# Performance work log

Measured on AMD Instinct MI355X. Metric: run time of the kernel, lower is better.

Reference implementation:

```python
import jax, jax.numpy as jnp
import numpy as np

S_LEN, T_LEN, BATCH, HID = 32, 32, 64, 512


def setup_inputs() -> dict:
    key = jax.random.key(0)
    ks = jax.random.split(key, 5)
    H = HID
    sc = lambda n: 1.0 / np.sqrt(n)
    return {
        "source": jax.random.normal(ks[0], (S_LEN, BATCH, H), jnp.float32),
        "target": jax.random.normal(ks[1], (T_LEN, BATCH, H), jnp.float32),
        # H2h Dense: concat(s_h, t_h) [B, 2H] -> [B, H], linear
        "W_H2h": (jax.random.normal(ks[2], (2 * H, H), jnp.float32) * sc(2 * H)),
        "b_H2h": jnp.zeros((H,), jnp.float32),
        # shared LSTMCell weights (Keras gate order i, f, g, o)
        "W_kernel": (jax.random.normal(ks[3], (H, 4 * H), jnp.float32) * sc(H)),
        "W_rec": (jax.random.normal(ks[4], (H, 4 * H), jnp.float32) * sc(H)),
        "b_lstm": jnp.zeros((4 * H,), jnp.float32),
    }


def _lstm_cell(x, h, c, Wk, Wr, b):
    # Keras LSTMCell math, gate order i, f, g(candidate), o
    z = x @ Wk + h @ Wr + b  # [B, 4H]
    i, f, g, o = jnp.split(z, 4, axis=-1)
    c2 = jax.nn.sigmoid(f) * c + jax.nn.sigmoid(i) * jnp.tanh(g)
    h2 = jax.nn.sigmoid(o) * jnp.tanh(c2)
    return h2, c2


def reference(source, target, W_H2h, b_H2h, W_kernel, W_rec, b_lstm):
    # source: [S, B, H] (time-major), target: [T, B, H]
    T, B, H = target.shape

    def inner(s_state, t_slice):
        # s_state carried along the target axis; t_slice is target cell j state
        s_step, s_h, s_m = s_state
        t_step, t_h, t_m = t_slice
        hmid = jnp.concatenate([s_h, t_h], axis=1) @ W_H2h + b_H2h  # [B, H]
        ns_h, ns_m = _lstm_cell(s_step, hmid, s_m, W_kernel, W_rec, b_lstm)
        nt_h, nt_m = _lstm_cell(t_step, hmid, t_m, W_kernel, W_rec, b_lstm)
        # step arrays get overwritten with the new hidden state
        return (ns_h, ns_h, ns_m), (nt_h, nt_h, nt_m)

    def outer(t_arrays, s_in):
        # fresh source state per outer step i: step = source[i], h = m = 0
        z = jnp.zeros_like(s_in)
        (s_step_f, _, _), t_new = jax.lax.scan(inner, (s_in, z, z), t_arrays)
        return t_new, s_step_f

    zeros = jnp.zeros((T, B, H), source.dtype)
    t_final, source_out = jax.lax.scan(outer, (target, zeros, zeros), source)
    return source_out, t_final[0]
```

## Files before the change

kernel.cpp:

```cpp
#include <hip/hip_runtime.h>

#define BLK 256

typedef __bf16 bf16;
typedef __bf16 bf16x8 __attribute__((ext_vector_type(8)));
typedef float f32x4 __attribute__((ext_vector_type(4)));

__device__ __forceinline__ float sigm(float x) { return 1.f / (1.f + __expf(-x)); }
__device__ __forceinline__ float tanh_(float x) {
    x = fminf(fmaxf(x, -15.f), 15.f);
    float e = __expf(2.f * x);
    return (e - 1.f) / (e + 1.f);
}

__device__ __forceinline__ void gl2lds(const bf16* g, bf16* l) {
    __builtin_amdgcn_global_load_lds((const __attribute__((address_space(1))) void*)g,
                                     (__attribute__((address_space(3))) void*)l, 16, 0, 0);
}

__global__ __launch_bounds__(256) void k_prep(
    const float* __restrict__ src, const float* __restrict__ tgt,
    const float* __restrict__ WH, const float* __restrict__ bH,
    const float* __restrict__ Wk, const float* __restrict__ Wr,
    const float* __restrict__ bl,
    bf16* __restrict__ srcb, bf16* __restrict__ tgtb,
    bf16* __restrict__ WHhi, bf16* __restrict__ WHlo,
    bf16* __restrict__ Wrhi, bf16* __restrict__ Wrlo,
    bf16* __restrict__ P2, float* __restrict__ bz) {
    __shared__ float tile[64][65];
    const int bid = blockIdx.x, t = threadIdx.x;
    if (bid < 512) {
        const float* in = (bid < 256) ? Wr : Wk;
        bf16* ohi = (bid < 256) ? Wrhi : P2;
        bf16* olo = (bid < 256) ? Wrlo : nullptr;
        const int b = bid & 255;
        const int tr = b >> 5, tc = b & 31;
#pragma unroll
        for (int q = 0; q < 16; q++) {
            int idx = q * 256 + t, lr = idx >> 6, lc = idx & 63;
            tile[lr][lc] = in[(size_t)(tr * 64 + lr) * 2048 + tc * 64 + lc];
        }
        __syncthreads();
#pragma unroll
        for (int q = 0; q < 16; q++) {
            int idx = q * 256 + t, lr = idx >> 6, lc = idx & 63;
            float v = tile[lc][lr];
            size_t o = (size_t)(tc * 64 + lr) * 512 + tr * 64 + lc;
            bf16 h = (bf16)v;
            ohi[o] = h;
            if (olo) olo[o] = (bf16)(v - (float)h);
        }
    } else if (bid < 520) {
        int c = (bid - 512) * 256 + t;
        float s = bl[c];
        for (int k = 0; k < 512; k++) s += bH[k] * Wr[(size_t)k * 2048 + c];
        bz[c] = s;
    } else {
        const int gt = (bid - 520) * 256 + t, NT = 504 * 256;
        for (int id = gt; id < 1048576; id += NT) srcb[id] = (bf16)src[id];
        for (int id = gt; id < 1048576; id += NT) tgtb[id] = (bf16)tgt[id];
        for (int id = gt; id < 524288; id += NT) {
            float v = WH[id];
            bf16 h = (bf16)v;
            WHhi[id] = h;
            WHlo[id] = (bf16)(v - (float)h);
        }
    }
}

__global__ __launch_bounds__(256, 4) void k_gemmP(
    const bf16* __restrict__ Wrhi, const bf16* __restrict__ Wrlo,
    const bf16* __restrict__ WHhi, const bf16* __restrict__ WHlo,
    const float* __restrict__ Wk,
    bf16* __restrict__ P1, bf16* __restrict__ P3,
    bf16* __restrict__ P4, bf16* __restrict__ P5) {
    __shared__ __align__(16) bf16 At[64 * 64];
    __shared__ __align__(16) bf16 Bt[128 * 64];
    const int t = threadIdx.x, w = t >> 6, l = t & 63;
    const int m0 = (blockIdx.x >> 3) * 64, n0 = (blockIdx.x & 7) * 128;
    f32x4 acc[2][4] = {};
    const bf16* Aps[3] = {Wrhi, Wrlo, Wrhi};
    const bf16* Bps[3] = {WHhi, WHhi, WHlo};
    for (int ph = 0; ph < 3; ph++) {
        const bf16* Ap = Aps[ph] + (size_t)m0 * 512;
        const bf16* Bp = Bps[ph] + (size_t)n0 * 512;
        for (int kt = 0; kt < 8; kt++) {
            int k0 = kt * 64;
            __syncthreads();
#pragma unroll
            for (int q = 0; q < 2; q++) {
                int pp = q * 256 + t;
                int r = pp >> 3, c = (pp & 7) ^ (r & 7);
                gl2lds(Ap + (size_t)r * 512 + k0 + c * 8, &At[(q * 256 + w * 64) * 8]);
            }
#pragma unroll
            for (int q = 0; q < 4; q++) {
                int pp = q * 256 + t;
                int r = pp >> 3, c = (pp & 7) ^ (r & 7);
                gl2lds(Bp + (size_t)r * 512 + k0 + c * 8, &Bt[(q * 256 + w * 64) * 8]);
            }
            __syncthreads();
#pragma unroll
            for (int ks = 0; ks < 2; ks++) {
                int c = ks * 4 + (l >> 4);
                bf16x8 af[2], bb[4];
#pragma unroll
                for (int mt = 0; mt < 2; mt++) {
                    int r = (w >> 1) * 32 + mt * 16 + (l & 15);
                    af[mt] = *(const bf16x8*)&At[(r * 8 + (c ^ (r & 7))) * 8];
                }
#pragma unroll
                for (int g = 0; g < 4; g++) {
                    int r = g * 32 + (w & 1) * 16 + (l & 15);
                    bb[g] = *(const bf16x8*)&Bt[(r * 8 + (c ^ (r & 7))) * 8];
                }
#pragma unroll
                for (int mt = 0; mt < 2; mt++)
#pragma unroll
                    for (int g = 0; g < 4; g++)
                        acc[mt][g] = __builtin_amdgcn_mfma_f32_16x16x32_bf16(
                            af[mt], bb[g], acc[mt][g], 0, 0, 0);
            }
        }
    }
    const bool hihalf = (n0 >= 512);
#pragma unroll
    for (int mt = 0; mt < 2; mt++) {
#pragma unroll
        for (int g = 0; g < 4; g++) {
            int np = n0 + g * 32 + (w & 1) * 16 + (l & 15);
#pragma unroll
            for (int r = 0; r < 4; r++) {
                int c = m0 + (w >> 1) * 32 + mt * 16 + ((l >> 4) << 2) + r;
                float v = acc[mt][g][r];
                if (!hihalf) {
                    P4[(size_t)c * 512 + np] = (bf16)v;
                    P1[(size_t)c * 512 + np] = (bf16)(v + Wk[(size_t)np * 2048 + c]);
                } else {
                    int kk = np - 512;
                    P3[(size_t)c * 512 + kk] = (bf16)v;
                    P5[(size_t)c * 512 + kk] = (bf16)(v + Wk[(size_t)kk * 2048 + c]);
                }
            }
        }
    }
}

__global__ __launch_bounds__(256, 3) void k_diag3(
    int d, int i_lo,
    const bf16* __restrict__ srcb, const bf16* __restrict__ tgtb,
    const bf16* __restrict__ P1, const bf16* __restrict__ P2,
    const bf16* __restrict__ P3, const bf16* __restrict__ P4,
    const bf16* __restrict__ P5,
    const float* __restrict__ bz,
    const bf16* __restrict__ shR, bf16* __restrict__ shW,
    const bf16* __restrict__ thR, bf16* __restrict__ thW,
    float* __restrict__ sc, float* __restrict__ tc,
    float* __restrict__ out) {
    __shared__ __align__(16) bf16 At[64 * 128];
    __shared__ __align__(16) bf16 Bt[128 * 128];
    const int t = threadIdx.x, w = t >> 6, l = t & 63;
    const int cell = blockIdx.x >> 5, sub = blockIdx.x & 31;
    const int side = sub >> 4, ch0 = (sub & 15) << 5;
    const int i = i_lo + cell, j = d - i;
    const size_t stI = (size_t)i * 32768, stJ = (size_t)j * 32768;

    const bf16* Ah[2];
    const bf16* Wh[2];
    int nh = 0;
    if (side == 0) {
        Ah[nh] = (j == 0 ? srcb : shR) + stI;
        Wh[nh] = (j == 0 ? P2 : P1);
        nh++;
        if (i > 0) { Ah[nh] = thR + stJ; Wh[nh] = P3; nh++; }
    } else {
        if (j > 0) { Ah[nh] = shR + stI; Wh[nh] = P4; nh++; }
        Ah[nh] = (i == 0 ? tgtb : thR) + stJ;
        Wh[nh] = (i == 0 ? P2 : P5);
        nh++;
    }

    f32x4 acc[2][4] = {};
    for (int hh = 0; hh < nh; hh++) {
        const bf16* Ap = Ah[hh];
        const bf16* Wp = Wh[hh];
#pragma unroll 1
        for (int kt = 0; kt < 4; kt++) {
            int k0 = kt * 128;
            __syncthreads();
#pragma unroll
            for (int q = 0; q < 4; q++) {
                int pp = q * 256 + t;
                int r = pp >> 4, c = (pp & 15) ^ (r & 15);
                gl2lds(Ap + (size_t)r * 512 + k0 + c * 8, &At[(q * 256 + w * 64) * 8]);
            }
#pragma unroll
            for (int q = 0; q < 8; q++) {
                int pp = q * 256 + t;
                int r = pp >> 4, c = (pp & 15) ^ (r & 15);
                int g = r >> 5;
                gl2lds(Wp + (size_t)(g * 512 + ch0 + (r & 31)) * 512 + k0 + c * 8,
                       &Bt[(q * 256 + w * 64) * 8]);
            }
            __syncthreads();
#pragma unroll
            for (int ks = 0; ks < 4; ks++) {
                int cq = ks * 4 + (l >> 4);
                bf16x8 af[2], bb[4];
#pragma unroll
                for (int mt = 0; mt < 2; mt++) {
                    int r = (w >> 1) * 32 + mt * 16 + (l & 15);
                    af[mt] = *(const bf16x8*)&At[(r * 16 + (cq ^ (r & 15))) * 8];
                }
#pragma unroll
                for (int g = 0; g < 4; g++) {
                    int r = g * 32 + (w & 1) * 16 + (l & 15);
                    bb[g] = *(const bf16x8*)&Bt[(r * 16 + (cq ^ (r & 15))) * 8];
                }
#pragma unroll
                for (int mt = 0; mt < 2; mt++)
#pragma unroll
                    for (int g = 0; g < 4; g++)
                        acc[mt][g] = __builtin_amdgcn_mfma_f32_16x16x32_bf16(
                            af[mt], bb[g], acc[mt][g], 0, 0, 0);
            }
        }
    }

    const int h = ch0 + (w & 1) * 16 + (l & 15);
    float bzv[4];
#pragma unroll
    for (int g = 0; g < 4; g++) bzv[g] = bz[g * 512 + h];
#pragma unroll
    for (int mt = 0; mt < 2; mt++) {
#pragma unroll
        for (int r = 0; r < 4; r++) {
            int b = (w >> 1) * 32 + mt * 16 + ((l >> 4) << 2) + r;
            float zi = acc[mt][0][r] + bzv[0];
            float zf = acc[mt][1][r] + bzv[1];
            float zg = acc[mt][2][r] + bzv[2];
            float zo = acc[mt][3][r] + bzv[3];
            if (side == 0) {
                size_t off = stI + (size_t)b * 512 + h;
                float cold = (j == 0) ? 0.f : sc[off];
                float c2 = sigm(zf) * cold + sigm(zi) * tanh_(zg);
                float h2 = sigm(zo) * tanh_(c2);
                sc[off] = c2;
                shW[off] = (bf16)h2;
                if (j == 31) out[off] = h2;
            } else {
                size_t off = stJ + (size_t)b * 512 + h;
                float cold = (i == 0) ? 0.f : tc[off];
                float c2 = sigm(zf) * cold + sigm(zi) * tanh_(zg);
                float h2 = sigm(zo) * tanh_(c2);
                tc[off] = c2;
                thW[off] = (bf16)h2;
                if (i == 31) out[1048576 + off] = h2;
            }
        }
    }
}


extern "C" void kernel_launch(void* const* d_in, const int* in_sizes, int n_in,
                              void* d_out, int out_size, void* d_ws, size_t ws_size,
                              hipStream_t stream) {
    char* w = (char*)d_ws;
    const size_t MB = 1u << 20;
    const float* src = (const float*)d_in[0];
    const float* tgt = (const float*)d_in[1];
    const float* WH = (const float*)d_in[2];
    const float* bH = (const float*)d_in[3];
    const float* Wk = (const float*)d_in[4];
    const float* Wr = (const float*)d_in[5];
    const float* bl = (const float*)d_in[6];
    float* out = (float*)d_out;

    bf16* srcb = (bf16*)(w + 0 * MB);
    bf16* tgtb = (bf16*)(w + 2 * MB);
    bf16* WHhi = (bf16*)(w + 4 * MB);
    bf16* WHlo = (bf16*)(w + 5 * MB);
    bf16* Wrhi = (bf16*)(w + 6 * MB);
    bf16* Wrlo = (bf16*)(w + 8 * MB);
    bf16* P1 = (bf16*)(w + 10 * MB);
    bf16* P2 = (bf16*)(w + 12 * MB);
    bf16* P3 = (bf16*)(w + 14 * MB);
    bf16* P4 = (bf16*)(w + 16 * MB);
    bf16* P5 = (bf16*)(w + 18 * MB);
    float* bz = (float*)(w + 20 * MB);
    bf16* sh = (bf16*)(w + 21 * MB);
    bf16* th = (bf16*)(w + 25 * MB);
    float* sc = (float*)(w + 29 * MB);
    float* tc = (float*)(w + 33 * MB);

    k_prep<<<1024, BLK, 0, stream>>>(src, tgt, WH, bH, Wk, Wr, bl, srcb, tgtb,
                                     WHhi, WHlo, Wrhi, Wrlo, P2, bz);
    k_gemmP<<<256, BLK, 0, stream>>>(Wrhi, Wrlo, WHhi, WHlo, Wk, P1, P3, P4, P5);

    for (int d = 0; d < 63; d++) {
        int i_lo = d > 31 ? d - 31 : 0;
        int i_hi = d < 31 ? d : 31;
        int Kd = i_hi - i_lo + 1;
        const bf16* shR = sh + (size_t)(d & 1) * 1048576;
        bf16* shW = sh + (size_t)((d + 1) & 1) * 1048576;
        const bf16* thR = th + (size_t)(d & 1) * 1048576;
        bf16* thW = th + (size_t)((d + 1) & 1) * 1048576;
        k_diag3<<<Kd * 32, BLK, 0, stream>>>(d, i_lo, srcb, tgtb, P1, P2, P3, P4, P5,
                                             bz, shR, shW, thR, thW, sc, tc, out);
    }
}
```

Before: 1.410 ms.

## Load A operand directly to registers and add deep-K variant for small diagonals

The diagonal kernel no longer stages the activation tile in LDS. Each wave reads its A fragments straight from global memory into registers, which cuts LDS use and raises the occupancy hint to 4. A second kernel variant uses a 256-wide K tile with a larger LDS weight buffer, so short diagonals with few blocks go through fewer K iterations and barriers. The host picks a variant per diagonal by its cell count. Direct global A loads read each row without the LDS reuse across waves, and they add register pressure.

```diff
diff --git a/kernel.cpp b/kernel.cpp
--- a/kernel.cpp
+++ b/kernel.cpp
@@ -146,88 +146,36 @@
     }
 }
 
-__global__ __launch_bounds__(256, 3) void k_diag3(
-    int d, int i_lo,
-    const bf16* __restrict__ srcb, const bf16* __restrict__ tgtb,
-    const bf16* __restrict__ P1, const bf16* __restrict__ P2,
-    const bf16* __restrict__ P3, const bf16* __restrict__ P4,
-    const bf16* __restrict__ P5,
-    const float* __restrict__ bz,
-    const bf16* __restrict__ shR, bf16* __restrict__ shW,
-    const bf16* __restrict__ thR, bf16* __restrict__ thW,
-    float* __restrict__ sc, float* __restrict__ tc,
-    float* __restrict__ out) {
-    __shared__ __align__(16) bf16 At[64 * 128];
-    __shared__ __align__(16) bf16 Bt[128 * 128];
-    const int t = threadIdx.x, w = t >> 6, l = t & 63;
-    const int cell = blockIdx.x >> 5, sub = blockIdx.x & 31;
-    const int side = sub >> 4, ch0 = (sub & 15) << 5;
-    const int i = i_lo + cell, j = d - i;
+__device__ __forceinline__ int build_panels(int i, int d, int side,
+                                            const bf16* srcb, const bf16* tgtb,
+                                            const bf16* shR, const bf16* thR,
+                                            const bf16* P1, const bf16* P2,
+                                            const bf16* P3, const bf16* P4,
+                                            const bf16* P5, const bf16** A,
+                                            const bf16** W) {
+    const int j = d - i;
     const size_t stI = (size_t)i * 32768, stJ = (size_t)j * 32768;
-
-    const bf16* Ah[2];
-    const bf16* Wh[2];
     int nh = 0;
     if (side == 0) {
-        Ah[nh] = (j == 0 ? srcb : shR) + stI;
-        Wh[nh] = (j == 0 ? P2 : P1);
+        A[nh] = (j == 0 ? srcb : shR) + stI;
+        W[nh] = (j == 0 ? P2 : P1);
         nh++;
-        if (i > 0) { Ah[nh] = thR + stJ; Wh[nh] = P3; nh++; }
+        if (i > 0) { A[nh] = thR + stJ; W[nh] = P3; nh++; }
     } else {
-        if (j > 0) { Ah[nh] = shR + stI; Wh[nh] = P4; nh++; }
-        Ah[nh] = (i == 0 ? tgtb : thR) + stJ;
-        Wh[nh] = (i == 0 ? P2 : P5);
+        if (j > 0) { A[nh] = shR + stI; W[nh] = P4; nh++; }
+        A[nh] = (i == 0 ? tgtb : thR) + stJ;
+        W[nh] = (i == 0 ? P2 : P5);
         nh++;
     }
-
-    f32x4 acc[2][4] = {};
-    for (int hh = 0; hh < nh; hh++) {
-        const bf16* Ap = Ah[hh];
-        const bf16* Wp = Wh[hh];
-#pragma unroll 1
-        for (int kt = 0; kt < 4; kt++) {
-            int k0 = kt * 128;
-            __syncthreads();
-#pragma unroll
-            for (int q = 0; q < 4; q++) {
-                int pp = q * 256 + t;
-                int r = pp >> 4, c = (pp & 15) ^ (r & 15);
-                gl2lds(Ap + (size_t)r * 512 + k0 + c * 8, &At[(q * 256 + w * 64) * 8]);
-            }
-#pragma unroll
-            for (int q = 0; q < 8; q++) {
-                int pp = q * 256 + t;
-                int r = pp >> 4, c = (pp & 15) ^ (r & 15);
-                int g = r >> 5;
-                gl2lds(Wp + (size_t)(g * 512 + ch0 + (r & 31)) * 512 + k0 + c * 8,
-                       &Bt[(q * 256 + w * 64) * 8]);
-            }
-            __syncthreads();
-#pragma unroll
-            for (int ks = 0; ks < 4; ks++) {
-                int cq = ks * 4 + (l >> 4);
-                bf16x8 af[2], bb[4];
-#pragma unroll
-                for (int mt = 0; mt < 2; mt++) {
-                    int r = (w >> 1) * 32 + mt * 16 + (l & 15);
-                    af[mt] = *(const bf16x8*)&At[(r * 16 + (cq ^ (r & 15))) * 8];
-                }
-#pragma unroll
-                for (int g = 0; g < 4; g++) {
-                    int r = g * 32 + (w & 1) * 16 + (l & 15);
-                    bb[g] = *(const bf16x8*)&Bt[(r * 16 + (cq ^ (r & 15))) * 8];
-                }
-#pragma unroll
-                for (int mt = 0; mt < 2; mt++)
-#pragma unroll
-                    for (int g = 0; g < 4; g++)
-                        acc[mt][g] = __builtin_amdgcn_mfma_f32_16x16x32_bf16(
-                            af[mt], bb[g], acc[mt][g], 0, 0, 0);
-            }
-        }
-    }
-
-    const int h = ch0 + (w & 1) * 16 + (l & 15);
+    return nh;
+}
+
+__device__ __forceinline__ void epilogue(int i, int j, int side, int h, int w, int l,
+                                         const float* __restrict__ bz,
+                                         f32x4 (*acc)[4], float* __restrict__ sc,
+                                         float* __restrict__ tc, bf16* __restrict__ shW,
+                                         bf16* __restrict__ thW, float* __restrict__ out) {
+    const size_t stI = (size_t)i * 32768, stJ = (size_t)j * 32768;
     float bzv[4];
 #pragma unroll
     for (int g = 0; g < 4; g++) bzv[g] = bz[g * 512 + h];
@@ -261,6 +209,142 @@
     }
 }
 
+__global__ __launch_bounds__(256, 4) void k_diagV(
+    int d, int i_lo,
+    const bf16* __restrict__ srcb, const bf16* __restrict__ tgtb,
+    const bf16* __restrict__ P1, const bf16* __restrict__ P2,
+    const bf16* __restrict__ P3, const bf16* __restrict__ P4,
+    const bf16* __restrict__ P5,
+    const float* __restrict__ bz,
+    const bf16* __restrict__ shR, bf16* __restrict__ shW,
+    const bf16* __restrict__ thR, bf16* __restrict__ thW,
+    float* __restrict__ sc, float* __restrict__ tc,
+    float* __restrict__ out) {
+    __shared__ __align__(16) bf16 Bt[128 * 128];
+    const int t = threadIdx.x, w = t >> 6, l = t & 63;
+    const int cell = blockIdx.x >> 5, sub = blockIdx.x & 31;
+    const int side = sub >> 4, ch0 = (sub & 15) << 5;
+    const int i = i_lo + cell, j = d - i;
+
+    const bf16 *Ah[2], *Wh[2];
+    const int nh = build_panels(i, d, side, srcb, tgtb, shR, thR, P1, P2, P3, P4, P5, Ah, Wh);
+
+    f32x4 acc[2][4] = {};
+    for (int hh = 0; hh < nh; hh++) {
+        const bf16* Ap = Ah[hh];
+        const bf16* Wp = Wh[hh];
+#pragma unroll 1
+        for (int kt = 0; kt < 4; kt++) {
+            int k0 = kt * 128;
+            __syncthreads();
+#pragma unroll
+            for (int q = 0; q < 8; q++) {
+                int pp = q * 256 + t;
+                int r = pp >> 4, c = (pp & 15) ^ (r & 15);
+                int g = r >> 5;
+                gl2lds(Wp + (size_t)(g * 512 + ch0 + (r & 31)) * 512 + k0 + c * 8,
+                       &Bt[(q * 256 + w * 64) * 8]);
+            }
+            bf16x8 af[2][4];
+#pragma unroll
+            for (int mt = 0; mt < 2; mt++) {
+                int r = (w >> 1) * 32 + mt * 16 + (l & 15);
+                const bf16* ap = Ap + (size_t)r * 512 + k0 + (l >> 4) * 8;
+#pragma unroll
+                for (int ks = 0; ks < 4; ks++) af[mt][ks] = *(const bf16x8*)(ap + ks * 32);
+            }
+            __syncthreads();
+#pragma unroll
+            for (int ks = 0; ks < 4; ks++) {
+                int cq = ks * 4 + (l >> 4);
+                bf16x8 bb[4];
+#pragma unroll
+                for (int g = 0; g < 4; g++) {
+                    int r = g * 32 + (w & 1) * 16 + (l & 15);
+                    bb[g] = *(const bf16x8*)&Bt[(r * 16 + (cq ^ (r & 15))) * 8];
+                }
+#pragma unroll
+                for (int mt = 0; mt < 2; mt++)
+#pragma unroll
+                    for (int g = 0; g < 4; g++)
+                        acc[mt][g] = __builtin_amdgcn_mfma_f32_16x16x32_bf16(
+                            af[mt][ks], bb[g], acc[mt][g], 0, 0, 0);
+            }
+        }
+    }
+
+    const int h = ch0 + (w & 1) * 16 + (l & 15);
+    epilogue(i, j, side, h, w, l, bz, acc, sc, tc, shW, thW, out);
+}
+
+__global__ __launch_bounds__(256, 2) void k_diagS(
+    int d, int i_lo,
+    const bf16* __restrict__ srcb, const bf16* __restrict__ tgtb,
+    const bf16* __restrict__ P1, const bf16* __restrict__ P2,
+    const bf16* __restrict__ P3, const bf16* __restrict__ P4,
+    const bf16* __restrict__ P5,
+    const float* __restrict__ bz,
+    const bf16* __restrict__ shR, bf16* __restrict__ shW,
+    const bf16* __restrict__ thR, bf16* __restrict__ thW,
+    float* __restrict__ sc, float* __restrict__ tc,
+    float* __restrict__ out) {
+    __shared__ __align__(16) bf16 Bt[128 * 256];
+    const int t = threadIdx.x, w = t >> 6, l = t & 63;
+    const int cell = blockIdx.x >> 5, sub = blockIdx.x & 31;
+    const int side = sub >> 4, ch0 = (sub & 15) << 5;
+    const int i = i_lo + cell, j = d - i;
+
+    const bf16 *Ah[2], *Wh[2];
+    const int nh = build_panels(i, d, side, srcb, tgtb, shR, thR, P1, P2, P3, P4, P5, Ah, Wh);
+
+    f32x4 acc[2][4] = {};
+    for (int hh = 0; hh < nh; hh++) {
+        const bf16* Ap = Ah[hh];
+        const bf16* Wp = Wh[hh];
+#pragma unroll 1
+        for (int kt = 0; kt < 2; kt++) {
+            int k0 = kt * 256;
+            __syncthreads();
+#pragma unroll
+            for (int q = 0; q < 16; q++) {
+                int pp = q * 256 + t;
+                int r = pp >> 5, c = (pp & 31) ^ (r & 31);
+                int g = r >> 5;
+                gl2lds(Wp + (size_t)(g * 512 + ch0 + (r & 31)) * 512 + k0 + c * 8,
+                       &Bt[(q * 256 + w * 64) * 8]);
+            }
+            bf16x8 af[2][8];
+#pragma unroll
+            for (int mt = 0; mt < 2; mt++) {
+                int r = (w >> 1) * 32 + mt * 16 + (l & 15);
+                const bf16* ap = Ap + (size_t)r * 512 + k0 + (l >> 4) * 8;
+#pragma unroll
+                for (int ks = 0; ks < 8; ks++) af[mt][ks] = *(const bf16x8*)(ap + ks * 32);
+            }
+            __syncthreads();
+#pragma unroll
+            for (int ks = 0; ks < 8; ks++) {
+                int cq = ks * 4 + (l >> 4);
+                bf16x8 bb[4];
+#pragma unroll
+                for (int g = 0; g < 4; g++) {
+                    int r = g * 32 + (w & 1) * 16 + (l & 15);
+                    bb[g] = *(const bf16x8*)&Bt[(r * 32 + (cq ^ (r & 31))) * 8];
+                }
+#pragma unroll
+                for (int mt = 0; mt < 2; mt++)
+#pragma unroll
+                    for (int g = 0; g < 4; g++)
+                        acc[mt][g] = __builtin_amdgcn_mfma_f32_16x16x32_bf16(
+                            af[mt][ks], bb[g], acc[mt][g], 0, 0, 0);
+            }
+        }
+    }
+
+    const int h = ch0 + (w & 1) * 16 + (l & 15);
+    epilogue(i, j, side, h, w, l, bz, acc, sc, tc, shW, thW, out);
+}
+
 
 extern "C" void kernel_launch(void* const* d_in, const int* in_sizes, int n_in,
                               void* d_out, int out_size, void* d_ws, size_t ws_size,
@@ -305,7 +389,14 @@
         bf16* shW = sh + (size_t)((d + 1) & 1) * 1048576;
         const bf16* thR = th + (size_t)(d & 1) * 1048576;
         bf16* thW = th + (size_t)((d + 1) & 1) * 1048576;
-        k_diag3<<<Kd * 32, BLK, 0, stream>>>(d, i_lo, srcb, tgtb, P1, P2, P3, P4, P5,
-                                             bz, shR, shW, thR, thW, sc, tc, out);
-    }
-}
+        if (Kd > 8) {
+            k_diagV<<<Kd * 32, BLK, 0, stream>>>(d, i_lo, srcb, tgtb, P1, P2, P3, P4,
+                                                 P5, bz, shR, shW, thR, thW, sc, tc,
+                                                 out);
+        } else {
+            k_diagS<<<Kd * 32, BLK, 0, stream>>>(d, i_lo, srcb, tgtb, P1, P2, P3, P4,
+                                                 P5, bz, shR, shW, thR, thW, sc, tc,
+                                                 out);
+        }
+    }
+}
```

New measurement: 2.258 ms. +60.2%, slower.

## Schedule diagonal jobs via XCD-affine atomic queues for weight L2 locality

Applied to the files above, without the earlier changes.

Each block of the per-diagonal kernel now takes its job from one of eight atomic counters, starting with the queue matching its XCD id and stealing from others when that queue is empty. Jobs in a queue share the same output-channel slices, so each XCD mostly reads a fixed subset of the weight panels and can keep them in its own L2. The counters are zeroed inside the prep kernel. This adds one atomic and one barrier per block, and the speedup depends on the hardware scheduler spreading blocks evenly across XCDs.

```diff
diff --git a/kernel.cpp b/kernel.cpp
--- a/kernel.cpp
+++ b/kernel.cpp
@@ -16,6 +16,26 @@
 __device__ __forceinline__ void gl2lds(const bf16* g, bf16* l) {
     __builtin_amdgcn_global_load_lds((const __attribute__((address_space(1))) void*)g,
                                      (__attribute__((address_space(3))) void*)l, 16, 0, 0);
+}
+
+__device__ __forceinline__ int xcd_id() {
+    int x;
+    asm volatile("s_getreg_b32 %0, hwreg(HW_REG_XCC_ID)" : "=s"(x));
+    return x & 7;
+}
+
+__device__ __forceinline__ int pop_job(int* cnt, int Kd4, int t, int* jobSlot) {
+    if (t == 0) {
+        int got = -1, x = xcd_id();
+        for (int k = 0; k < 8 && got < 0; k++) {
+            int q = (x + k) & 7;
+            int idx = atomicAdd(&cnt[q], 1);
+            if (idx < Kd4) got = (idx << 3) | q;
+        }
+        *jobSlot = got;
+    }
+    __syncthreads();
+    return *jobSlot;
 }
 
 __global__ __launch_bounds__(256) void k_prep(
@@ -26,7 +46,7 @@
     bf16* __restrict__ srcb, bf16* __restrict__ tgtb,
     bf16* __restrict__ WHhi, bf16* __restrict__ WHlo,
     bf16* __restrict__ Wrhi, bf16* __restrict__ Wrlo,
-    bf16* __restrict__ P2, float* __restrict__ bz) {
+    bf16* __restrict__ P2, float* __restrict__ bz, int* __restrict__ qcnt) {
     __shared__ float tile[64][65];
     const int bid = blockIdx.x, t = threadIdx.x;
     if (bid < 512) {
@@ -65,6 +85,7 @@
             WHhi[id] = h;
             WHlo[id] = (bf16)(v - (float)h);
         }
+        for (int id = gt; id < 512; id += NT) qcnt[id] = 0;
     }
 }
 
@@ -146,88 +167,36 @@
     }
 }
 
-__global__ __launch_bounds__(256, 3) void k_diag3(
-    int d, int i_lo,
-    const bf16* __restrict__ srcb, const bf16* __restrict__ tgtb,
-    const bf16* __restrict__ P1, const bf16* __restrict__ P2,
-    const bf16* __restrict__ P3, const bf16* __restrict__ P4,
-    const bf16* __restrict__ P5,
-    const float* __restrict__ bz,
-    const bf16* __restrict__ shR, bf16* __restrict__ shW,
-    const bf16* __restrict__ thR, bf16* __restrict__ thW,
-    float* __restrict__ sc, float* __restrict__ tc,
-    float* __restrict__ out) {
-    __shared__ __align__(16) bf16 At[64 * 128];
-    __shared__ __align__(16) bf16 Bt[128 * 128];
-    const int t = threadIdx.x, w = t >> 6, l = t & 63;
-    const int cell = blockIdx.x >> 5, sub = blockIdx.x & 31;
-    const int side = sub >> 4, ch0 = (sub & 15) << 5;
-    const int i = i_lo + cell, j = d - i;
+__device__ __forceinline__ int build_panels(int i, int d, int side,
+                                            const bf16* srcb, const bf16* tgtb,
+                                            const bf16* shR, const bf16* thR,
+                                            const bf16* P1, const bf16* P2,
+                                            const bf16* P3, const bf16* P4,
+                                            const bf16* P5, const bf16** A,
+                                            const bf16** W) {
+    const int j = d - i;
     const size_t stI = (size_t)i * 32768, stJ = (size_t)j * 32768;
-
-    const bf16* Ah[2];
-    const bf16* Wh[2];
     int nh = 0;
     if (side == 0) {
-        Ah[nh] = (j == 0 ? srcb : shR) + stI;
-        Wh[nh] = (j == 0 ? P2 : P1);
+        A[nh] = (j == 0 ? srcb : shR) + stI;
+        W[nh] = (j == 0 ? P2 : P1);
         nh++;
-        if (i > 0) { Ah[nh] = thR + stJ; Wh[nh] = P3; nh++; }
+        if (i > 0) { A[nh] = thR + stJ; W[nh] = P3; nh++; }
     } else {
-        if (j > 0) { Ah[nh] = shR + stI; Wh[nh] = P4; nh++; }
-        Ah[nh] = (i == 0 ? tgtb : thR) + stJ;
-        Wh[nh] = (i == 0 ? P2 : P5);
+        if (j > 0) { A[nh] = shR + stI; W[nh] = P4; nh++; }
+        A[nh] = (i == 0 ? tgtb : thR) + stJ;
+        W[nh] = (i == 0 ? P2 : P5);
         nh++;
     }
-
-    f32x4 acc[2][4] = {};
-    for (int hh = 0; hh < nh; hh++) {
-        const bf16* Ap = Ah[hh];
-        const bf16* Wp = Wh[hh];
-#pragma unroll 1
-        for (int kt = 0; kt < 4; kt++) {
-            int k0 = kt * 128;
-            __syncthreads();
-#pragma unroll
-            for (int q = 0; q < 4; q++) {
-                int pp = q * 256 + t;
-                int r = pp >> 4, c = (pp & 15) ^ (r & 15);
-                gl2lds(Ap + (size_t)r * 512 + k0 + c * 8, &At[(q * 256 + w * 64) * 8]);
-            }
-#pragma unroll
-            for (int q = 0; q < 8; q++) {
-                int pp = q * 256 + t;
-                int r = pp >> 4, c = (pp & 15) ^ (r & 15);
-                int g = r >> 5;
-                gl2lds(Wp + (size_t)(g * 512 + ch0 + (r & 31)) * 512 + k0 + c * 8,
-                       &Bt[(q * 256 + w * 64) * 8]);
-            }
-            __syncthreads();
-#pragma unroll
-            for (int ks = 0; ks < 4; ks++) {
-                int cq = ks * 4 + (l >> 4);
-                bf16x8 af[2], bb[4];
-#pragma unroll
-                for (int mt = 0; mt < 2; mt++) {
-                    int r = (w >> 1) * 32 + mt * 16 + (l & 15);
-                    af[mt] = *(const bf16x8*)&At[(r * 16 + (cq ^ (r & 15))) * 8];
-                }
-#pragma unroll
-                for (int g = 0; g < 4; g++) {
-                    int r = g * 32 + (w & 1) * 16 + (l & 15);
-                    bb[g] = *(const bf16x8*)&Bt[(r * 16 + (cq ^ (r & 15))) * 8];
-                }
-#pragma unroll
-                for (int mt = 0; mt < 2; mt++)
-#pragma unroll
-                    for (int g = 0; g < 4; g++)
-                        acc[mt][g] = __builtin_amdgcn_mfma_f32_16x16x32_bf16(
-                            af[mt], bb[g], acc[mt][g], 0, 0, 0);
-            }
-        }
-    }
-
-    const int h = ch0 + (w & 1) * 16 + (l & 15);
+    return nh;
+}
+
+__device__ __forceinline__ void epilogue(int i, int j, int side, int h, int w, int l,
+                                         const float* __restrict__ bz,
+                                         f32x4 (*acc)[4], float* __restrict__ sc,
+                                         float* __restrict__ tc, bf16* __restrict__ shW,
+                                         bf16* __restrict__ thW, float* __restrict__ out) {
+    const size_t stI = (size_t)i * 32768, stJ = (size_t)j * 32768;
     float bzv[4];
 #pragma unroll
     for (int g = 0; g < 4; g++) bzv[g] = bz[g * 512 + h];
@@ -261,6 +230,84 @@
     }
 }
 
+__global__ __launch_bounds__(256, 3) void k_diag3(
+    int d, int i_lo, int Kd, int* __restrict__ qcnt,
+    const bf16* __restrict__ srcb, const bf16* __restrict__ tgtb,
+    const bf16* __restrict__ P1, const bf16* __restrict__ P2,
+    const bf16* __restrict__ P3, const bf16* __restrict__ P4,
+    const bf16* __restrict__ P5,
+    const float* __restrict__ bz,
+    const bf16* __restrict__ shR, bf16* __restrict__ shW,
+    const bf16* __restrict__ thR, bf16* __restrict__ thW,
+    float* __restrict__ sc, float* __restrict__ tc,
+    float* __restrict__ out) {
+    __shared__ __align__(16) bf16 At[64 * 128];
+    __shared__ __align__(16) bf16 Bt[128 * 128];
+    __shared__ int jobSlot;
+    const int t = threadIdx.x, w = t >> 6, l = t & 63;
+
+    const int job = pop_job(qcnt, Kd * 4, t, &jobSlot);
+    if (job < 0) return;
+    const int sub = (job & 7) * 4 + ((job >> 3) & 3);
+    const int cell = job >> 5;
+
+    const int side = sub >> 4, ch0 = (sub & 15) << 5;
+    const int i = i_lo + cell, j = d - i;
+
+    const bf16 *Ah[2], *Wh[2];
+    const int nh = build_panels(i, d, side, srcb, tgtb, shR, thR, P1, P2, P3, P4, P5, Ah, Wh);
+
+    f32x4 acc[2][4] = {};
+    for (int hh = 0; hh < nh; hh++) {
+        const bf16* Ap = Ah[hh];
+        const bf16* Wp = Wh[hh];
+#pragma unroll 1
+        for (int kt = 0; kt < 4; kt++) {
+            int k0 = kt * 128;
+            __syncthreads();
+#pragma unroll
+            for (int q = 0; q < 4; q++) {
+                int pp = q * 256 + t;
+                int r = pp >> 4, c = (pp & 15) ^ (r & 15);
+                gl2lds(Ap + (size_t)r * 512 + k0 + c * 8, &At[(q * 256 + w * 64) * 8]);
+            }
+#pragma unroll
+            for (int q = 0; q < 8; q++) {
+                int pp = q * 256 + t;
+                int r = pp >> 4, c = (pp & 15) ^ (r & 15);
+                int g = r >> 5;
+                gl2lds(Wp + (size_t)(g * 512 + ch0 + (r & 31)) * 512 + k0 + c * 8,
+                       &Bt[(q * 256 + w * 64) * 8]);
+            }
+            __syncthreads();
+#pragma unroll
+            for (int ks = 0; ks < 4; ks++) {
+                int cq = ks * 4 + (l >> 4);
+                bf16x8 af[2], bb[4];
+#pragma unroll
+                for (int mt = 0; mt < 2; mt++) {
+                    int r = (w >> 1) * 32 + mt * 16 + (l & 15);
+                    af[mt] = *(const bf16x8*)&At[(r * 16 + (cq ^ (r & 15))) * 8];
+                }
+#pragma unroll
+                for (int g = 0; g < 4; g++) {
+                    int r = g * 32 + (w & 1) * 16 + (l & 15);
+                    bb[g] = *(const bf16x8*)&Bt[(r * 16 + (cq ^ (r & 15))) * 8];
+                }
+#pragma unroll
+                for (int mt = 0; mt < 2; mt++)
+#pragma unroll
+                    for (int g = 0; g < 4; g++)
+                        acc[mt][g] = __builtin_amdgcn_mfma_f32_16x16x32_bf16(
+                            af[mt], bb[g], acc[mt][g], 0, 0, 0);
+            }
+        }
+    }
+
+    const int h = ch0 + (w & 1) * 16 + (l & 15);
+    epilogue(i, j, side, h, w, l, bz, acc, sc, tc, shW, thW, out);
+}
+
 
 extern "C" void kernel_launch(void* const* d_in, const int* in_sizes, int n_in,
                               void* d_out, int out_size, void* d_ws, size_t ws_size,
@@ -292,9 +339,10 @@
     bf16* th = (bf16*)(w + 25 * MB);
     float* sc = (float*)(w + 29 * MB);
     float* tc = (float*)(w + 33 * MB);
+    int* qcnt = (int*)(w + 37 * MB);
 
     k_prep<<<1024, BLK, 0, stream>>>(src, tgt, WH, bH, Wk, Wr, bl, srcb, tgtb,
-                                     WHhi, WHlo, Wrhi, Wrlo, P2, bz);
+                                     WHhi, WHlo, Wrhi, Wrlo, P2, bz, qcnt);
     k_gemmP<<<256, BLK, 0, stream>>>(Wrhi, Wrlo, WHhi, WHlo, Wk, P1, P3, P4, P5);
 
     for (int d = 0; d < 63; d++) {
@@ -305,7 +353,8 @@
         bf16* shW = sh + (size_t)((d + 1) & 1) * 1048576;
         const bf16* thR = th + (size_t)(d & 1) * 1048576;
         bf16* thW = th + (size_t)((d + 1) & 1) * 1048576;
-        k_diag3<<<Kd * 32, BLK, 0, stream>>>(d, i_lo, srcb, tgtb, P1, P2, P3, P4, P5,
-                                             bz, shR, shW, thR, thW, sc, tc, out);
-    }
-}
+        k_diag3<<<Kd * 32, BLK, 0, stream>>>(d, i_lo, Kd, qcnt + d * 8, srcb, tgtb,
+                                             P1, P2, P3, P4, P5, bz, shR, shW, thR,
+                                             thW, sc, tc, out);
+    }
+}
```

New measurement: 2.806 ms. +99.1%, slower.
